# Kernel optimization log

Hardware: AMD Instinct MI355X
Metric: run time of the kernel (lower is better)

Reference implementation:

```python
import jax, jax.numpy as jnp
import numpy as np
from jax import lax

EPS = 1e-5
B = 512

def _conv(x, w, pad):
    # x: [B,Cin,H,W], w: [Cout,Cin,kh,kw]
    return lax.conv_general_dilated(x, w, (1, 1), [(pad, pad), (pad, pad)],
                                    dimension_numbers=('NCHW', 'OIHW', 'NCHW'))

def _bn2d(x, g, b, m, v):
    s = g * lax.rsqrt(v + EPS)
    return x * s[None, :, None, None] + (b - m * s)[None, :, None, None]

def _bn1d(x, g, b, m, v):
    s = g * lax.rsqrt(v + EPS)
    return x * s + (b - m * s)

def _pool2(x):
    return lax.reduce_window(x, -jnp.inf, lax.max, (1, 1, 2, 2), (1, 1, 2, 2), 'VALID')

def setup_inputs() -> dict:
    key = jax.random.key(0)
    ks = iter(jax.random.split(key, 64))
    rn = lambda shape, s=1.0: jax.random.normal(next(ks), shape, dtype=jnp.float32) * s
    un = lambda shape: jax.random.uniform(next(ks), shape, dtype=jnp.float32, minval=0.5, maxval=1.5)
    def bn_params(c):
        return (jnp.ones((c,), jnp.float32), jnp.zeros((c,), jnp.float32), rn((c,), 0.1), un((c,)))
    inp = {"x": rn((B, 3, 64, 64))}
    inp["w1"] = rn((32, 3, 5, 5), 0.1)
    inp["bn1_g"], inp["bn1_b"], inp["bn1_m"], inp["bn1_v"] = bn_params(32)
    inp["w2"] = rn((64, 32, 3, 3), 0.06)
    inp["bn2_g"], inp["bn2_b"], inp["bn2_m"], inp["bn2_v"] = bn_params(64)
    inp["w3"] = rn((128, 64, 3, 3), 0.04)
    inp["bn3_g"], inp["bn3_b"], inp["bn3_m"], inp["bn3_v"] = bn_params(128)
    inp["fc_w"] = rn((256, 8192), 0.01)
    inp["fc_b"] = jnp.zeros((256,), jnp.float32)
    inp["bnf_g"], inp["bnf_b"], inp["bnf_m"], inp["bnf_v"] = bn_params(256)
    inp["c_w1"] = rn((64, 256), 0.06)
    inp["c_b1"] = jnp.zeros((64,), jnp.float32)
    inp["bnc_g"], inp["bnc_b"], inp["bnc_m"], inp["bnc_v"] = bn_params(64)
    inp["c_w2"] = rn((1, 64), 0.1)
    inp["c_b2"] = jnp.zeros((1,), jnp.float32)
    inp["m_w1"] = rn((64, 256), 0.06)
    inp["m_b1"] = jnp.zeros((64,), jnp.float32)
    inp["bnm_g"], inp["bnm_b"], inp["bnm_m"], inp["bnm_v"] = bn_params(64)
    inp["m_w2"] = rn((1, 64), 0.1)
    inp["m_b2"] = jnp.zeros((1,), jnp.float32)
    return inp

def reference(x, w1, bn1_g, bn1_b, bn1_m, bn1_v,
              w2, bn2_g, bn2_b, bn2_m, bn2_v,
              w3, bn3_g, bn3_b, bn3_m, bn3_v,
              fc_w, fc_b, bnf_g, bnf_b, bnf_m, bnf_v,
              c_w1, c_b1, bnc_g, bnc_b, bnc_m, bnc_v, c_w2, c_b2,
              m_w1, m_b1, bnm_g, bnm_b, bnm_m, bnm_v, m_w2, m_b2):
    # Block 1: conv5x5(3->32) + BN + ReLU + maxpool2 -> [B,32,32,32]
    h = _pool2(jax.nn.relu(_bn2d(_conv(x, w1, 2), bn1_g, bn1_b, bn1_m, bn1_v)))
    # Block 2: conv3x3(32->64) + BN + ReLU + maxpool2 -> [B,64,16,16]
    h = _pool2(jax.nn.relu(_bn2d(_conv(h, w2, 1), bn2_g, bn2_b, bn2_m, bn2_v)))
    # Block 3: conv3x3(64->128) + BN + ReLU + maxpool2 + ToDense -> [B,128,8,8]
    h = _pool2(jax.nn.relu(_bn2d(_conv(h, w3, 1), bn3_g, bn3_b, bn3_m, bn3_v)))
    f = h.reshape(h.shape[0], -1)  # [B, 8192]
    s = jax.nn.relu(_bn1d(f @ fc_w.T + fc_b, bnf_g, bnf_b, bnf_m, bnf_v))  # [B,256]
    c = jax.nn.relu(_bn1d(s @ c_w1.T + c_b1, bnc_g, bnc_b, bnc_m, bnc_v)) @ c_w2.T + c_b2
    mo = jax.nn.relu(_bn1d(s @ m_w1.T + m_b1, bnm_g, bnm_b, bnm_m, bnm_v)) @ m_w2.T + m_b2
    return (c, mo)  # ([B,1], [B,1])
```

## Files before the change

kernel.cpp:

```cpp
#include <hip/hip_runtime.h>
#include <hip/hip_bf16.h>

#define EPS 1e-5f

typedef __attribute__((ext_vector_type(8))) short bf16x8;
typedef __attribute__((ext_vector_type(4))) float f32x4;

__device__ __forceinline__ ushort f2b(float f) {
    return __builtin_bit_cast(ushort, __float2bfloat16(f));
}
__device__ __forceinline__ bf16x8 ld_frag(const char* p) {
    return __builtin_bit_cast(bf16x8, *reinterpret_cast<const uint4*>(p));
}

__global__ __launch_bounds__(256) void k_prep_all(
    const float* __restrict__ w1, const float* __restrict__ w2,
    const float* __restrict__ w3, const float* __restrict__ fcw,
    const float* __restrict__ x,
    ushort* __restrict__ w1p, ushort* __restrict__ w2p, ushort* __restrict__ w3p,
    ushort* __restrict__ fcwp, ushort* __restrict__ x4p,
    ushort* __restrict__ h1p, ushort* __restrict__ h2p)
{
    __shared__ ushort l[128 * 66];
    const int bid = blockIdx.x, t = threadIdx.x;
    if (bid < 128) {
        const int total = 5120 + 18432 + 73728;
        for (int i = bid * 256 + t; i < total; i += 128 * 256) {
            if (i < 5120) {
                const int ky = i >> 10, co = (i >> 5) & 31, k = i & 31;
                const int kx = k >> 2, ci = k & 3;
                float v = 0.f;
                if (kx < 5 && ci < 3) v = w1[((co * 3 + ci) * 5 + ky) * 5 + kx];
                w1p[i] = f2b(v);
            } else if (i < 5120 + 18432) {
                const int j = i - 5120;
                const int tap = j >> 11, co = (j >> 5) & 63, ci = j & 31;
                w2p[j] = f2b(w2[(co * 32 + ci) * 9 + tap]);
            } else {
                const int j = i - (5120 + 18432);
                const int tap = j >> 13, co = (j >> 6) & 127, ci = j & 63;
                w3p[j] = f2b(w3[(co * 64 + ci) * 9 + tap]);
            }
        }
    } else if (bid < 384) {
        const int j = bid - 128;
        const float* src = fcw + (size_t)j * 8192;
        #pragma unroll
        for (int i = 0; i < 32; ++i) {
            const int idx = i * 256 + t;
            const int c = idx >> 6, p = idx & 63;
            l[c * 66 + p] = f2b(src[idx]);
        }
        __syncthreads();
        ushort* dst = fcwp + (size_t)j * 8192;
        #pragma unroll
        for (int i = 0; i < 32; ++i) {
            const int idx = i * 256 + t;
            const int c = idx & 127, p = idx >> 7;
            dst[idx] = l[c * 66 + p];
        }
    } else if (bid < 4480) {
        for (int p = (bid - 384) * 256 + t; p < 2506752; p += 4096 * 256) {
            const int n = p / 4896;
            const int rem = p - n * 4896;
            const int row = rem / 72, col = rem - row * 72;
            const int gr = row - 2, gc = col - 2;
            ushort4 pk; pk.x = 0; pk.y = 0; pk.z = 0; pk.w = 0;
            if ((unsigned)gr < 64u && (unsigned)gc < 64u) {
                const size_t base = ((size_t)n * 3 << 12) + (gr << 6) + gc;
                pk.x = f2b(x[base]); pk.y = f2b(x[base + 4096]); pk.z = f2b(x[base + 8192]);
            }
            *reinterpret_cast<ushort4*>(&x4p[(size_t)p * 4]) = pk;
        }
    } else if (bid < 4736) {
        const uint4 z = {0, 0, 0, 0};
        for (int i = (bid - 4480) * 256 + t; i < 270336; i += 256 * 256) {
            const int img = i / 528;
            const int rem = i - img * 528;
            const int px = rem >> 2, gg = rem & 3;
            int row, col;
            if (px < 34)      { row = 0;  col = px; }
            else if (px < 68) { row = 33; col = px - 34; }
            else { const int q = px - 68; row = 1 + (q >> 1); col = (q & 1) ? 33 : 0; }
            *reinterpret_cast<uint4*>(&h1p[(((size_t)img * 34 + row) * 34 + col) * 32 + gg * 8]) = z;
        }
    } else if (bid < 4992) {
        const uint4 z = {0, 0, 0, 0};
        for (int i = (bid - 4736) * 256 + t; i < 278528; i += 256 * 256) {
            const int img = i / 544;
            const int rem = i - img * 544;
            const int px = rem >> 3, gg = rem & 7;
            int row, col;
            if (px < 18)      { row = 0;  col = px; }
            else if (px < 36) { row = 17; col = px - 18; }
            else { const int q = px - 36; row = 1 + (q >> 1); col = (q & 1) ? 17 : 0; }
            *reinterpret_cast<uint4*>(&h2p[(((size_t)img * 18 + row) * 18 + col) * 64 + gg * 8]) = z;
        }
    }
}

__global__ __launch_bounds__(256) void k_conv1(
    const ushort* __restrict__ x4p, const ushort* __restrict__ w1p,
    const float* __restrict__ bg, const float* __restrict__ bb,
    const float* __restrict__ bm, const float* __restrict__ bv,
    ushort* __restrict__ h1p)
{
    __shared__ __align__(16) ushort xs[12 * 72 * 4];
    __shared__ __align__(16) ushort ws[5 * 32 * 32];
    const int bid = blockIdx.x;
    const int n = bid >> 3, q = bid & 7;
    const int t = threadIdx.x;
    const int wave = t >> 6, lane = t & 63;
    const int g = lane >> 4, l15 = lane & 15;

    {
        const ushort* src = x4p + ((size_t)(n * 68 + 8 * q) * 72) * 4;
        for (int i = t; i < 432; i += 256)
            *reinterpret_cast<uint4*>(&xs[i * 8]) = *reinterpret_cast<const uint4*>(src + i * 8);
    }
    for (int i = t; i < 640; i += 256) {
        const int gg = i & 3, r = i >> 2;
        const int co = r & 31;
        const uint4 v = *reinterpret_cast<const uint4*>(&w1p[r * 32 + gg * 8]);
        *reinterpret_cast<uint4*>((char*)ws + r * 64 + ((gg ^ ((co >> 1) & 3)) << 4)) = v;
    }
    __syncthreads();

    f32x4 acc[8][2];
    #pragma unroll
    for (int i = 0; i < 8; ++i) { acc[i][0] = (f32x4){0,0,0,0}; acc[i][1] = (f32x4){0,0,0,0}; }

    const char* xsb = (const char*)xs;
    const char* wsb = (const char*)ws;
    #pragma unroll
    for (int ky = 0; ky < 5; ++ky) {
        bf16x8 a[8], b[2];
        #pragma unroll
        for (int mt = 0; mt < 8; ++mt) {
            const int crl = 2 * wave + (mt >> 2);
            const int ccl = (mt & 3) * 16 + l15;
            const int off = ((crl + ky) * 72 + ccl) * 8 + g * 16;
            const uint2 lo = *reinterpret_cast<const uint2*>(xsb + off);
            const uint2 hi = *reinterpret_cast<const uint2*>(xsb + off + 8);
            uint4 all; all.x = lo.x; all.y = lo.y; all.z = hi.x; all.w = hi.y;
            a[mt] = __builtin_bit_cast(bf16x8, all);
        }
        #pragma unroll
        for (int nt = 0; nt < 2; ++nt) {
            const int co = nt * 16 + l15;
            b[nt] = ld_frag(wsb + (ky * 32 + co) * 64 + ((g ^ ((co >> 1) & 3)) << 4));
        }
        #pragma unroll
        for (int mt = 0; mt < 8; ++mt)
            #pragma unroll
            for (int nt = 0; nt < 2; ++nt)
                acc[mt][nt] = __builtin_amdgcn_mfma_f32_16x16x32_bf16(a[mt], b[nt], acc[mt][nt], 0, 0, 0);
    }

    const int prow = q * 4 + wave;
    #pragma unroll
    for (int nt = 0; nt < 2; ++nt) {
        const int co = nt * 16 + l15;
        const float s = bg[co] * rsqrtf(bv[co] + EPS);
        const float bsv = bb[co] - bm[co] * s;
        #pragma unroll
        for (int mt = 0; mt < 4; ++mt) {
            #pragma unroll
            for (int j = 0; j < 2; ++j) {
                const float v0 = fmaxf(fmaf(acc[mt][nt][2 * j],     s, bsv), 0.f);
                const float v1 = fmaxf(fmaf(acc[mt][nt][2 * j + 1], s, bsv), 0.f);
                const float v2 = fmaxf(fmaf(acc[mt + 4][nt][2 * j],     s, bsv), 0.f);
                const float v3 = fmaxf(fmaf(acc[mt + 4][nt][2 * j + 1], s, bsv), 0.f);
                const int ppc = mt * 8 + g * 2 + j;
                h1p[(((size_t)n * 34 + prow + 1) * 34 + ppc + 1) * 32 + co] =
                    f2b(fmaxf(fmaxf(v0, v1), fmaxf(v2, v3)));
            }
        }
    }
}

__global__ __launch_bounds__(256, 2) void k_conv2(
    const ushort* __restrict__ h1p, const ushort* __restrict__ w2p,
    const float* __restrict__ bg, const float* __restrict__ bb,
    const float* __restrict__ bm, const float* __restrict__ bv,
    ushort* __restrict__ h2p)
{
    __shared__ __align__(16) ushort xs[10 * 34 * 32];
    __shared__ __align__(16) ushort ws[9 * 64 * 32];
    const int bid = blockIdx.x;
    const int ngrp = bid >> 2, q = bid & 3;
    const int t = threadIdx.x;
    const int wave = t >> 6, lane = t & 63;
    const int g = lane >> 4, l15 = lane & 15;
    const char* xsb = (const char*)xs;
    const char* wsb = (const char*)ws;

    for (int i = t; i < 2304; i += 256) {
        const int gg = i & 3, r = i >> 2;
        const int co = r & 63;
        const uint4 v = *reinterpret_cast<const uint4*>(&w2p[r * 32 + gg * 8]);
        *reinterpret_cast<uint4*>((char*)ws + r * 64 + ((gg ^ ((co >> 1) & 3)) << 4)) = v;
    }

    for (int img = 0; img < 4; ++img) {
        const int n = ngrp * 4 + img;
        if (img) __syncthreads();
        {
            const ushort* src = h1p + ((size_t)(n * 34 + 8 * q) * 34) * 32;
            for (int i = t; i < 1360; i += 256) {
                const int gg = i & 3, pix = i >> 2;
                const uint4 v = *reinterpret_cast<const uint4*>(src + i * 8);
                *reinterpret_cast<uint4*>((char*)xs + pix * 64 + ((gg ^ ((pix >> 1) & 3)) << 4)) = v;
            }
        }
        __syncthreads();

        f32x4 acc[4][4];
        #pragma unroll
        for (int i = 0; i < 4; ++i)
            #pragma unroll
            for (int j = 0; j < 4; ++j) acc[i][j] = (f32x4){0,0,0,0};

        #pragma unroll
        for (int tap = 0; tap < 9; ++tap) {
            const int ky = tap / 3, kx = tap - 3 * ky;
            bf16x8 a[4], b[4];
            #pragma unroll
            for (int mt = 0; mt < 4; ++mt) {
                const int crl = 2 * wave + (mt >> 1);
                const int ccl = (mt & 1) * 16 + l15;
                const int pix = (crl + ky) * 34 + ccl + kx;
                a[mt] = ld_frag(xsb + pix * 64 + ((g ^ ((pix >> 1) & 3)) << 4));
            }
            #pragma unroll
            for (int nt = 0; nt < 4; ++nt) {
                const int co = nt * 16 + l15;
                b[nt] = ld_frag(wsb + (tap * 64 + co) * 64 + ((g ^ ((co >> 1) & 3)) << 4));
            }
            #pragma unroll
            for (int mt = 0; mt < 4; ++mt)
                #pragma unroll
                for (int nt = 0; nt < 4; ++nt)
                    acc[mt][nt] = __builtin_amdgcn_mfma_f32_16x16x32_bf16(a[mt], b[nt], acc[mt][nt], 0, 0, 0);
        }

        const int prow = q * 4 + wave;
        #pragma unroll
        for (int nt = 0; nt < 4; ++nt) {
            const int co = nt * 16 + l15;
            const float s = bg[co] * rsqrtf(bv[co] + EPS);
            const float bsv = bb[co] - bm[co] * s;
            #pragma unroll
            for (int mtl = 0; mtl < 2; ++mtl) {
                #pragma unroll
                for (int j = 0; j < 2; ++j) {
                    const float v0 = fmaxf(fmaf(acc[mtl][nt][2 * j],     s, bsv), 0.f);
                    const float v1 = fmaxf(fmaf(acc[mtl][nt][2 * j + 1], s, bsv), 0.f);
                    const float v2 = fmaxf(fmaf(acc[mtl + 2][nt][2 * j],     s, bsv), 0.f);
                    const float v3 = fmaxf(fmaf(acc[mtl + 2][nt][2 * j + 1], s, bsv), 0.f);
                    const int ppc = mtl * 8 + g * 2 + j;
                    h2p[(((size_t)n * 18 + prow + 1) * 18 + ppc + 1) * 64 + co] =
                        f2b(fmaxf(fmaxf(v0, v1), fmaxf(v2, v3)));
                }
            }
        }
    }
}

__global__ __launch_bounds__(256, 2) void k_conv3(
    const ushort* __restrict__ h2p, const ushort* __restrict__ w3p,
    const float* __restrict__ bg, const float* __restrict__ bb,
    const float* __restrict__ bm, const float* __restrict__ bv,
    ushort* __restrict__ h3)
{
    __shared__ __align__(16) ushort xs[2 * 324 * 32];
    __shared__ __align__(16) ushort ws[9 * 64 * 32];
    const int bid = blockIdx.x;
    const int ngrp = bid >> 1, ch = bid & 1;
    const int t = threadIdx.x;
    const int wave = t >> 6, lane = t & 63;
    const int wl = wave & 1, imgw = wave >> 1;
    const int n = ngrp * 2 + imgw;
    const int g = lane >> 4, l15 = lane & 15;
    const char* xsb = (const char*)xs;
    const char* wsb = (const char*)ws;

    f32x4 acc[8][4];
    #pragma unroll
    for (int i = 0; i < 8; ++i)
        #pragma unroll
        for (int j = 0; j < 4; ++j) acc[i][j] = (f32x4){0,0,0,0};

    for (int gci = 0; gci < 2; ++gci) {
        if (gci) __syncthreads();
        for (int i = t; i < 2592; i += 256) {
            const int img2 = i / 1296;
            const int rem = i - img2 * 1296;
            const int pix = rem >> 2, gg = rem & 3;
            const int nsrc = ngrp * 2 + img2;
            const uint4 v = *reinterpret_cast<const uint4*>(
                &h2p[((size_t)nsrc * 324 + pix) * 64 + gci * 32 + gg * 8]);
            *reinterpret_cast<uint4*>((char*)xs + img2 * 20736 + pix * 64 +
                                      ((gg ^ ((pix >> 1) & 3)) << 4)) = v;
        }
        for (int i = t; i < 2304; i += 256) {
            const int gg = i & 3, r = i >> 2;
            const int tap = r >> 6, co = r & 63;
            const uint4 v = *reinterpret_cast<const uint4*>(
                &w3p[((size_t)(tap * 128 + ch * 64 + co) << 6) + gci * 32 + gg * 8]);
            *reinterpret_cast<uint4*>((char*)ws + r * 64 + ((gg ^ ((co >> 1) & 3)) << 4)) = v;
        }
        __syncthreads();
        #pragma unroll
        for (int tap = 0; tap < 9; ++tap) {
            const int ky = tap / 3, kx = tap - 3 * ky;
            bf16x8 a[8], b[4];
            #pragma unroll
            for (int mt = 0; mt < 8; ++mt) {
                const int pr = 8 * wl + mt;
                const int pix = (pr + ky) * 18 + l15 + kx;
                a[mt] = ld_frag(xsb + imgw * 20736 + pix * 64 + ((g ^ ((pix >> 1) & 3)) << 4));
            }
            #pragma unroll
            for (int nt = 0; nt < 4; ++nt) {
                const int co = nt * 16 + l15;
                b[nt] = ld_frag(wsb + (tap * 64 + co) * 64 + ((g ^ ((co >> 1) & 3)) << 4));
            }
            #pragma unroll
            for (int mt = 0; mt < 8; ++mt)
                #pragma unroll
                for (int nt = 0; nt < 4; ++nt)
                    acc[mt][nt] = __builtin_amdgcn_mfma_f32_16x16x32_bf16(a[mt], b[nt], acc[mt][nt], 0, 0, 0);
        }
    }

    #pragma unroll
    for (int nt = 0; nt < 4; ++nt) {
        const int co = ch * 64 + nt * 16 + l15;
        const float s = bg[co] * rsqrtf(bv[co] + EPS);
        const float bsv = bb[co] - bm[co] * s;
        #pragma unroll
        for (int k = 0; k < 4; ++k) {
            #pragma unroll
            for (int j = 0; j < 2; ++j) {
                const float v0 = fmaxf(fmaf(acc[2 * k][nt][2 * j],     s, bsv), 0.f);
                const float v1 = fmaxf(fmaf(acc[2 * k][nt][2 * j + 1], s, bsv), 0.f);
                const float v2 = fmaxf(fmaf(acc[2 * k + 1][nt][2 * j],     s, bsv), 0.f);
                const float v3 = fmaxf(fmaf(acc[2 * k + 1][nt][2 * j + 1], s, bsv), 0.f);
                const int ppr = 4 * wl + k;
                const int pcol = g * 2 + j;
                h3[(((size_t)n * 8 + ppr) * 8 + pcol) * 128 + co] =
                    f2b(fmaxf(fmaxf(v0, v1), fmaxf(v2, v3)));
            }
        }
    }
}

__global__ __launch_bounds__(256) void k_fc(
    const ushort* __restrict__ A, const ushort* __restrict__ Bw, float* __restrict__ C)
{
    __shared__ __align__(16) ushort As[64 * 32];
    __shared__ __align__(16) ushort Bs[64 * 32];
    const int bm = blockIdx.x, bn = blockIdx.y, kz = blockIdx.z;
    const int t = threadIdx.x;
    const int wave = t >> 6, lane = t & 63;
    const int g = lane >> 4, l15 = lane & 15;

    f32x4 acc[4];
    #pragma unroll
    for (int i = 0; i < 4; ++i) acc[i] = (f32x4){0,0,0,0};

    const char* asb = (const char*)As;
    const char* bsb = (const char*)Bs;
    for (int kk = 0; kk < 16; ++kk) {
        const int k0 = kz * 512 + kk * 32;
        if (kk) __syncthreads();
        {
            const int gg = t & 3, row = t >> 2;
            const uint4 va = *reinterpret_cast<const uint4*>(
                &A[(size_t)(bm * 64 + row) * 8192 + k0 + gg * 8]);
            *reinterpret_cast<uint4*>((char*)As + row * 64 + ((gg ^ ((row >> 1) & 3)) << 4)) = va;
            const uint4 vb = *reinterpret_cast<const uint4*>(
                &Bw[(size_t)(bn * 64 + row) * 8192 + k0 + gg * 8]);
            *reinterpret_cast<uint4*>((char*)Bs + row * 64 + ((gg ^ ((row >> 1) & 3)) << 4)) = vb;
        }
        __syncthreads();
        bf16x8 a[4], b;
        #pragma unroll
        for (int mt = 0; mt < 4; ++mt) {
            const int r = mt * 16 + l15;
            a[mt] = ld_frag(asb + r * 64 + ((g ^ ((r >> 1) & 3)) << 4));
        }
        {
            const int r = wave * 16 + l15;
            b = ld_frag(bsb + r * 64 + ((g ^ ((r >> 1) & 3)) << 4));
        }
        #pragma unroll
        for (int mt = 0; mt < 4; ++mt)
            acc[mt] = __builtin_amdgcn_mfma_f32_16x16x32_bf16(a[mt], b, acc[mt], 0, 0, 0);
    }

    float* Cp = C + (size_t)kz * 512 * 256;
    const int col = bn * 64 + wave * 16 + l15;
    #pragma unroll
    for (int mt = 0; mt < 4; ++mt) {
        #pragma unroll
        for (int r = 0; r < 4; ++r) {
            const int row = bm * 64 + mt * 16 + g * 4 + r;
            Cp[(size_t)row * 256 + col] = acc[mt][r];
        }
    }
}

__global__ __launch_bounds__(128) void k_heads(
    const float* __restrict__ sraw, const float* __restrict__ fcb,
    const float* __restrict__ fg, const float* __restrict__ fb,
    const float* __restrict__ fm, const float* __restrict__ fv,
    const float* __restrict__ cw1, const float* __restrict__ cb1,
    const float* __restrict__ cg, const float* __restrict__ cbb,
    const float* __restrict__ cm, const float* __restrict__ cv,
    const float* __restrict__ cw2, const float* __restrict__ cb2,
    const float* __restrict__ mw1, const float* __restrict__ mb1,
    const float* __restrict__ mg, const float* __restrict__ mbb,
    const float* __restrict__ mm, const float* __restrict__ mv,
    const float* __restrict__ mw2, const float* __restrict__ mb2,
    float* __restrict__ outp)
{
    __shared__ float sv[256];
    const int b = blockIdx.x, t = threadIdx.x;
    for (int k = t; k < 256; k += 128) {
        float val = fcb[k];
        #pragma unroll
        for (int z = 0; z < 16; ++z) val += sraw[(size_t)z * 131072 + b * 256 + k];
        const float s = fg[k] * rsqrtf(fv[k] + EPS);
        sv[k] = fmaxf(fmaf(val, s, fb[k] - fm[k] * s), 0.f);
    }
    __syncthreads();
    const int j = t & 63;
    const bool isM = (t >= 64);
    const float* w1  = isM ? mw1 : cw1;
    const float* b1  = isM ? mb1 : cb1;
    const float* g1  = isM ? mg  : cg;
    const float* bb1 = isM ? mbb : cbb;
    const float* m1  = isM ? mm  : cm;
    const float* v1  = isM ? mv  : cv;
    const float* w2  = isM ? mw2 : cw2;
    const float* b2  = isM ? mb2 : cb2;
    float d = 0.f;
    const float* wr = w1 + j * 256;
    #pragma unroll 8
    for (int k = 0; k < 256; ++k) d = fmaf(sv[k], wr[k], d);
    d += b1[j];
    const float s1 = g1[j] * rsqrtf(v1[j] + EPS);
    d = fmaxf(fmaf(d, s1, bb1[j] - m1[j] * s1), 0.f);
    float prod = d * w2[j];
    #pragma unroll
    for (int off = 32; off > 0; off >>= 1) prod += __shfl_down(prod, off);
    if (j == 0) outp[(isM ? 512 : 0) + b] = prod + b2[0];
}

extern "C" void kernel_launch(void* const* d_in, const int* in_sizes, int n_in,
                              void* d_out, int out_size, void* d_ws, size_t ws_size,
                              hipStream_t stream)
{
    const float* x    = (const float*)d_in[0];
    const float* w1   = (const float*)d_in[1];
    const float* bn1g = (const float*)d_in[2];
    const float* bn1b = (const float*)d_in[3];
    const float* bn1m = (const float*)d_in[4];
    const float* bn1v = (const float*)d_in[5];
    const float* w2   = (const float*)d_in[6];
    const float* bn2g = (const float*)d_in[7];
    const float* bn2b = (const float*)d_in[8];
    const float* bn2m = (const float*)d_in[9];
    const float* bn2v = (const float*)d_in[10];
    const float* w3   = (const float*)d_in[11];
    const float* bn3g = (const float*)d_in[12];
    const float* bn3b = (const float*)d_in[13];
    const float* bn3m = (const float*)d_in[14];
    const float* bn3v = (const float*)d_in[15];
    const float* fcw  = (const float*)d_in[16];
    const float* fcb  = (const float*)d_in[17];
    const float* bnfg = (const float*)d_in[18];
    const float* bnfb = (const float*)d_in[19];
    const float* bnfm = (const float*)d_in[20];
    const float* bnfv = (const float*)d_in[21];
    const float* cw1  = (const float*)d_in[22];
    const float* cb1  = (const float*)d_in[23];
    const float* bncg = (const float*)d_in[24];
    const float* bncb = (const float*)d_in[25];
    const float* bncm = (const float*)d_in[26];
    const float* bncv = (const float*)d_in[27];
    const float* cw2  = (const float*)d_in[28];
    const float* cb2  = (const float*)d_in[29];
    const float* mw1  = (const float*)d_in[30];
    const float* mb1  = (const float*)d_in[31];
    const float* bnmg = (const float*)d_in[32];
    const float* bnmb = (const float*)d_in[33];
    const float* bnmm = (const float*)d_in[34];
    const float* bnmv = (const float*)d_in[35];
    const float* mw2  = (const float*)d_in[36];
    const float* mb2  = (const float*)d_in[37];

    char* W = (char*)d_ws;
    ushort* x4p  = (ushort*)(W);
    ushort* h1p  = (ushort*)(W + 20054016);
    ushort* h2p  = (ushort*)(W + 57933824);
    ushort* h3   = (ushort*)(W + 79167488);
    ushort* w1p  = (ushort*)(W + 87556096);
    ushort* w2p  = (ushort*)(W + 87566336);
    ushort* w3p  = (ushort*)(W + 87603200);
    ushort* fcwp = (ushort*)(W + 87750656);
    float*  sr   = (float*) (W + 91944960);
    float* outp = (float*)d_out;

    k_prep_all<<<4992, 256, 0, stream>>>(w1, w2, w3, fcw, x,
                                         w1p, w2p, w3p, fcwp, x4p, h1p, h2p);
    k_conv1<<<512 * 8, 256, 0, stream>>>(x4p, w1p, bn1g, bn1b, bn1m, bn1v, h1p);
    k_conv2<<<128 * 4, 256, 0, stream>>>(h1p, w2p, bn2g, bn2b, bn2m, bn2v, h2p);
    k_conv3<<<256 * 2, 256, 0, stream>>>(h2p, w3p, bn3g, bn3b, bn3m, bn3v, h3);
    k_fc<<<dim3(8, 4, 16), 256, 0, stream>>>(h3, fcwp, sr);
    k_heads<<<512, 128, 0, stream>>>(sr, fcb, bnfg, bnfb, bnfm, bnfv,
                                     cw1, cb1, bncg, bncb, bncm, bncv, cw2, cb2,
                                     mw1, mb1, bnmg, bnmb, bnmm, bnmv, mw2, mb2, outp);
}
```

Before: 261.2 us.

## Drop LDS staging in conv kernels and load MFMA fragments from global

The three convolution kernels no longer stage input tiles and weights in shared memory. Each wave now loads its MFMA A and B fragments straight from global memory and relies on L1/L2 caching for reuse. conv2 and conv3 are restructured to handle one image per block, launching 4x and 2x more blocks, and launch bounds are raised to allow more resident blocks. This removes the LDS copy and barrier overhead in exchange for redundant global/cache traffic and possibly uncoalesced fragment loads.

```diff
diff --git a/kernel.cpp b/kernel.cpp
--- a/kernel.cpp
+++ b/kernel.cpp
@@ -9,7 +9,7 @@
 __device__ __forceinline__ ushort f2b(float f) {
     return __builtin_bit_cast(ushort, __float2bfloat16(f));
 }
-__device__ __forceinline__ bf16x8 ld_frag(const char* p) {
+__device__ __forceinline__ bf16x8 ld_frag(const void* p) {
     return __builtin_bit_cast(bf16x8, *reinterpret_cast<const uint4*>(p));
 }
 
@@ -99,56 +99,35 @@
     }
 }
 
-__global__ __launch_bounds__(256) void k_conv1(
+__global__ __launch_bounds__(256, 3) void k_conv1(
     const ushort* __restrict__ x4p, const ushort* __restrict__ w1p,
     const float* __restrict__ bg, const float* __restrict__ bb,
     const float* __restrict__ bm, const float* __restrict__ bv,
     ushort* __restrict__ h1p)
 {
-    __shared__ __align__(16) ushort xs[12 * 72 * 4];
-    __shared__ __align__(16) ushort ws[5 * 32 * 32];
     const int bid = blockIdx.x;
     const int n = bid >> 3, q = bid & 7;
     const int t = threadIdx.x;
     const int wave = t >> 6, lane = t & 63;
     const int g = lane >> 4, l15 = lane & 15;
 
-    {
-        const ushort* src = x4p + ((size_t)(n * 68 + 8 * q) * 72) * 4;
-        for (int i = t; i < 432; i += 256)
-            *reinterpret_cast<uint4*>(&xs[i * 8]) = *reinterpret_cast<const uint4*>(src + i * 8);
-    }
-    for (int i = t; i < 640; i += 256) {
-        const int gg = i & 3, r = i >> 2;
-        const int co = r & 31;
-        const uint4 v = *reinterpret_cast<const uint4*>(&w1p[r * 32 + gg * 8]);
-        *reinterpret_cast<uint4*>((char*)ws + r * 64 + ((gg ^ ((co >> 1) & 3)) << 4)) = v;
-    }
-    __syncthreads();
-
     f32x4 acc[8][2];
     #pragma unroll
     for (int i = 0; i < 8; ++i) { acc[i][0] = (f32x4){0,0,0,0}; acc[i][1] = (f32x4){0,0,0,0}; }
 
-    const char* xsb = (const char*)xs;
-    const char* wsb = (const char*)ws;
     #pragma unroll
     for (int ky = 0; ky < 5; ++ky) {
         bf16x8 a[8], b[2];
         #pragma unroll
         for (int mt = 0; mt < 8; ++mt) {
-            const int crl = 2 * wave + (mt >> 2);
-            const int ccl = (mt & 3) * 16 + l15;
-            const int off = ((crl + ky) * 72 + ccl) * 8 + g * 16;
-            const uint2 lo = *reinterpret_cast<const uint2*>(xsb + off);
-            const uint2 hi = *reinterpret_cast<const uint2*>(xsb + off + 8);
-            uint4 all; all.x = lo.x; all.y = lo.y; all.z = hi.x; all.w = hi.y;
-            a[mt] = __builtin_bit_cast(bf16x8, all);
+            const int cr = 8 * q + 2 * wave + (mt >> 2) + ky;
+            const int px = (mt & 3) * 16 + l15 + 2 * g;
+            a[mt] = ld_frag(&x4p[(((size_t)n * 68 + cr) * 72 + px) * 4]);
         }
         #pragma unroll
         for (int nt = 0; nt < 2; ++nt) {
             const int co = nt * 16 + l15;
-            b[nt] = ld_frag(wsb + (ky * 32 + co) * 64 + ((g ^ ((co >> 1) & 3)) << 4));
+            b[nt] = ld_frag(&w1p[(ky * 32 + co) * 32 + g * 8]);
         }
         #pragma unroll
         for (int mt = 0; mt < 8; ++mt)
@@ -179,63 +158,102 @@
     }
 }
 
-__global__ __launch_bounds__(256, 2) void k_conv2(
+__global__ __launch_bounds__(256, 4) void k_conv2(
     const ushort* __restrict__ h1p, const ushort* __restrict__ w2p,
     const float* __restrict__ bg, const float* __restrict__ bb,
     const float* __restrict__ bm, const float* __restrict__ bv,
     ushort* __restrict__ h2p)
 {
-    __shared__ __align__(16) ushort xs[10 * 34 * 32];
-    __shared__ __align__(16) ushort ws[9 * 64 * 32];
     const int bid = blockIdx.x;
-    const int ngrp = bid >> 2, q = bid & 3;
+    const int n = bid >> 2, q = bid & 3;
     const int t = threadIdx.x;
     const int wave = t >> 6, lane = t & 63;
     const int g = lane >> 4, l15 = lane & 15;
-    const char* xsb = (const char*)xs;
-    const char* wsb = (const char*)ws;
-
-    for (int i = t; i < 2304; i += 256) {
-        const int gg = i & 3, r = i >> 2;
-        const int co = r & 63;
-        const uint4 v = *reinterpret_cast<const uint4*>(&w2p[r * 32 + gg * 8]);
-        *reinterpret_cast<uint4*>((char*)ws + r * 64 + ((gg ^ ((co >> 1) & 3)) << 4)) = v;
-    }
-
-    for (int img = 0; img < 4; ++img) {
-        const int n = ngrp * 4 + img;
-        if (img) __syncthreads();
-        {
-            const ushort* src = h1p + ((size_t)(n * 34 + 8 * q) * 34) * 32;
-            for (int i = t; i < 1360; i += 256) {
-                const int gg = i & 3, pix = i >> 2;
-                const uint4 v = *reinterpret_cast<const uint4*>(src + i * 8);
-                *reinterpret_cast<uint4*>((char*)xs + pix * 64 + ((gg ^ ((pix >> 1) & 3)) << 4)) = v;
-            }
-        }
-        __syncthreads();
-
-        f32x4 acc[4][4];
-        #pragma unroll
-        for (int i = 0; i < 4; ++i)
-            #pragma unroll
-            for (int j = 0; j < 4; ++j) acc[i][j] = (f32x4){0,0,0,0};
-
+
+    f32x4 acc[4][4];
+    #pragma unroll
+    for (int i = 0; i < 4; ++i)
+        #pragma unroll
+        for (int j = 0; j < 4; ++j) acc[i][j] = (f32x4){0,0,0,0};
+
+    #pragma unroll
+    for (int tap = 0; tap < 9; ++tap) {
+        const int ky = tap / 3, kx = tap - 3 * ky;
+        bf16x8 a[4], b[4];
+        #pragma unroll
+        for (int mt = 0; mt < 4; ++mt) {
+            const int row = 8 * q + 2 * wave + (mt >> 1) + ky;
+            const int col = (mt & 1) * 16 + l15 + kx;
+            a[mt] = ld_frag(&h1p[(((size_t)n * 34 + row) * 34 + col) * 32 + g * 8]);
+        }
+        #pragma unroll
+        for (int nt = 0; nt < 4; ++nt) {
+            const int co = nt * 16 + l15;
+            b[nt] = ld_frag(&w2p[(tap * 64 + co) * 32 + g * 8]);
+        }
+        #pragma unroll
+        for (int mt = 0; mt < 4; ++mt)
+            #pragma unroll
+            for (int nt = 0; nt < 4; ++nt)
+                acc[mt][nt] = __builtin_amdgcn_mfma_f32_16x16x32_bf16(a[mt], b[nt], acc[mt][nt], 0, 0, 0);
+    }
+
+    const int prow = q * 4 + wave;
+    #pragma unroll
+    for (int nt = 0; nt < 4; ++nt) {
+        const int co = nt * 16 + l15;
+        const float s = bg[co] * rsqrtf(bv[co] + EPS);
+        const float bsv = bb[co] - bm[co] * s;
+        #pragma unroll
+        for (int mtl = 0; mtl < 2; ++mtl) {
+            #pragma unroll
+            for (int j = 0; j < 2; ++j) {
+                const float v0 = fmaxf(fmaf(acc[mtl][nt][2 * j],     s, bsv), 0.f);
+                const float v1 = fmaxf(fmaf(acc[mtl][nt][2 * j + 1], s, bsv), 0.f);
+                const float v2 = fmaxf(fmaf(acc[mtl + 2][nt][2 * j],     s, bsv), 0.f);
+                const float v3 = fmaxf(fmaf(acc[mtl + 2][nt][2 * j + 1], s, bsv), 0.f);
+                const int ppc = mtl * 8 + g * 2 + j;
+                h2p[(((size_t)n * 18 + prow + 1) * 18 + ppc + 1) * 64 + co] =
+                    f2b(fmaxf(fmaxf(v0, v1), fmaxf(v2, v3)));
+            }
+        }
+    }
+}
+
+__global__ __launch_bounds__(256, 4) void k_conv3(
+    const ushort* __restrict__ h2p, const ushort* __restrict__ w3p,
+    const float* __restrict__ bg, const float* __restrict__ bb,
+    const float* __restrict__ bm, const float* __restrict__ bv,
+    ushort* __restrict__ h3)
+{
+    const int bid = blockIdx.x;
+    const int n = bid >> 1, ch = bid & 1;
+    const int t = threadIdx.x;
+    const int wave = t >> 6, lane = t & 63;
+    const int g = lane >> 4, l15 = lane & 15;
+
+    f32x4 acc[4][4];
+    #pragma unroll
+    for (int i = 0; i < 4; ++i)
+        #pragma unroll
+        for (int j = 0; j < 4; ++j) acc[i][j] = (f32x4){0,0,0,0};
+
+    #pragma unroll
+    for (int gci = 0; gci < 2; ++gci) {
         #pragma unroll
         for (int tap = 0; tap < 9; ++tap) {
             const int ky = tap / 3, kx = tap - 3 * ky;
             bf16x8 a[4], b[4];
             #pragma unroll
             for (int mt = 0; mt < 4; ++mt) {
-                const int crl = 2 * wave + (mt >> 1);
-                const int ccl = (mt & 1) * 16 + l15;
-                const int pix = (crl + ky) * 34 + ccl + kx;
-                a[mt] = ld_frag(xsb + pix * 64 + ((g ^ ((pix >> 1) & 3)) << 4));
+                const int row = 4 * wave + mt + ky;
+                const int col = l15 + kx;
+                a[mt] = ld_frag(&h2p[(((size_t)n * 18 + row) * 18 + col) * 64 + gci * 32 + g * 8]);
             }
             #pragma unroll
             for (int nt = 0; nt < 4; ++nt) {
-                const int co = nt * 16 + l15;
-                b[nt] = ld_frag(wsb + (tap * 64 + co) * 64 + ((g ^ ((co >> 1) & 3)) << 4));
+                const int co = ch * 64 + nt * 16 + l15;
+                b[nt] = ld_frag(&w3p[((size_t)(tap * 128 + co)) * 64 + gci * 32 + g * 8]);
             }
             #pragma unroll
             for (int mt = 0; mt < 4; ++mt)
@@ -243,95 +261,6 @@
                 for (int nt = 0; nt < 4; ++nt)
                     acc[mt][nt] = __builtin_amdgcn_mfma_f32_16x16x32_bf16(a[mt], b[nt], acc[mt][nt], 0, 0, 0);
         }
-
-        const int prow = q * 4 + wave;
-        #pragma unroll
-        for (int nt = 0; nt < 4; ++nt) {
-            const int co = nt * 16 + l15;
-            const float s = bg[co] * rsqrtf(bv[co] + EPS);
-            const float bsv = bb[co] - bm[co] * s;
-            #pragma unroll
-            for (int mtl = 0; mtl < 2; ++mtl) {
-                #pragma unroll
-                for (int j = 0; j < 2; ++j) {
-                    const float v0 = fmaxf(fmaf(acc[mtl][nt][2 * j],     s, bsv), 0.f);
-                    const float v1 = fmaxf(fmaf(acc[mtl][nt][2 * j + 1], s, bsv), 0.f);
-                    const float v2 = fmaxf(fmaf(acc[mtl + 2][nt][2 * j],     s, bsv), 0.f);
-                    const float v3 = fmaxf(fmaf(acc[mtl + 2][nt][2 * j + 1], s, bsv), 0.f);
-                    const int ppc = mtl * 8 + g * 2 + j;
-                    h2p[(((size_t)n * 18 + prow + 1) * 18 + ppc + 1) * 64 + co] =
-                        f2b(fmaxf(fmaxf(v0, v1), fmaxf(v2, v3)));
-                }
-            }
-        }
-    }
-}
-
-__global__ __launch_bounds__(256, 2) void k_conv3(
-    const ushort* __restrict__ h2p, const ushort* __restrict__ w3p,
-    const float* __restrict__ bg, const float* __restrict__ bb,
-    const float* __restrict__ bm, const float* __restrict__ bv,
-    ushort* __restrict__ h3)
-{
-    __shared__ __align__(16) ushort xs[2 * 324 * 32];
-    __shared__ __align__(16) ushort ws[9 * 64 * 32];
-    const int bid = blockIdx.x;
-    const int ngrp = bid >> 1, ch = bid & 1;
-    const int t = threadIdx.x;
-    const int wave = t >> 6, lane = t & 63;
-    const int wl = wave & 1, imgw = wave >> 1;
-    const int n = ngrp * 2 + imgw;
-    const int g = lane >> 4, l15 = lane & 15;
-    const char* xsb = (const char*)xs;
-    const char* wsb = (const char*)ws;
-
-    f32x4 acc[8][4];
-    #pragma unroll
-    for (int i = 0; i < 8; ++i)
-        #pragma unroll
-        for (int j = 0; j < 4; ++j) acc[i][j] = (f32x4){0,0,0,0};
-
-    for (int gci = 0; gci < 2; ++gci) {
-        if (gci) __syncthreads();
-        for (int i = t; i < 2592; i += 256) {
-            const int img2 = i / 1296;
-            const int rem = i - img2 * 1296;
-            const int pix = rem >> 2, gg = rem & 3;
-            const int nsrc = ngrp * 2 + img2;
-            const uint4 v = *reinterpret_cast<const uint4*>(
-                &h2p[((size_t)nsrc * 324 + pix) * 64 + gci * 32 + gg * 8]);
-            *reinterpret_cast<uint4*>((char*)xs + img2 * 20736 + pix * 64 +
-                                      ((gg ^ ((pix >> 1) & 3)) << 4)) = v;
-        }
-        for (int i = t; i < 2304; i += 256) {
-            const int gg = i & 3, r = i >> 2;
-            const int tap = r >> 6, co = r & 63;
-            const uint4 v = *reinterpret_cast<const uint4*>(
-                &w3p[((size_t)(tap * 128 + ch * 64 + co) << 6) + gci * 32 + gg * 8]);
-            *reinterpret_cast<uint4*>((char*)ws + r * 64 + ((gg ^ ((co >> 1) & 3)) << 4)) = v;
-        }
-        __syncthreads();
-        #pragma unroll
-        for (int tap = 0; tap < 9; ++tap) {
-            const int ky = tap / 3, kx = tap - 3 * ky;
-            bf16x8 a[8], b[4];
-            #pragma unroll
-            for (int mt = 0; mt < 8; ++mt) {
-                const int pr = 8 * wl + mt;
-                const int pix = (pr + ky) * 18 + l15 + kx;
-                a[mt] = ld_frag(xsb + imgw * 20736 + pix * 64 + ((g ^ ((pix >> 1) & 3)) << 4));
-            }
-            #pragma unroll
-            for (int nt = 0; nt < 4; ++nt) {
-                const int co = nt * 16 + l15;
-                b[nt] = ld_frag(wsb + (tap * 64 + co) * 64 + ((g ^ ((co >> 1) & 3)) << 4));
-            }
-            #pragma unroll
-            for (int mt = 0; mt < 8; ++mt)
-                #pragma unroll
-                for (int nt = 0; nt < 4; ++nt)
-                    acc[mt][nt] = __builtin_amdgcn_mfma_f32_16x16x32_bf16(a[mt], b[nt], acc[mt][nt], 0, 0, 0);
-        }
     }
 
     #pragma unroll
@@ -340,14 +269,14 @@
         const float s = bg[co] * rsqrtf(bv[co] + EPS);
         const float bsv = bb[co] - bm[co] * s;
         #pragma unroll
-        for (int k = 0; k < 4; ++k) {
+        for (int k = 0; k < 2; ++k) {
             #pragma unroll
             for (int j = 0; j < 2; ++j) {
                 const float v0 = fmaxf(fmaf(acc[2 * k][nt][2 * j],     s, bsv), 0.f);
                 const float v1 = fmaxf(fmaf(acc[2 * k][nt][2 * j + 1], s, bsv), 0.f);
                 const float v2 = fmaxf(fmaf(acc[2 * k + 1][nt][2 * j],     s, bsv), 0.f);
                 const float v3 = fmaxf(fmaf(acc[2 * k + 1][nt][2 * j + 1], s, bsv), 0.f);
-                const int ppr = 4 * wl + k;
+                const int ppr = 2 * wave + k;
                 const int pcol = g * 2 + j;
                 h3[(((size_t)n * 8 + ppr) * 8 + pcol) * 128 + co] =
                     f2b(fmaxf(fmaxf(v0, v1), fmaxf(v2, v3)));
@@ -517,8 +446,8 @@
     k_prep_all<<<4992, 256, 0, stream>>>(w1, w2, w3, fcw, x,
                                          w1p, w2p, w3p, fcwp, x4p, h1p, h2p);
     k_conv1<<<512 * 8, 256, 0, stream>>>(x4p, w1p, bn1g, bn1b, bn1m, bn1v, h1p);
-    k_conv2<<<128 * 4, 256, 0, stream>>>(h1p, w2p, bn2g, bn2b, bn2m, bn2v, h2p);
-    k_conv3<<<256 * 2, 256, 0, stream>>>(h2p, w3p, bn3g, bn3b, bn3m, bn3v, h3);
+    k_conv2<<<512 * 4, 256, 0, stream>>>(h1p, w2p, bn2g, bn2b, bn2m, bn2v, h2p);
+    k_conv3<<<512 * 2, 256, 0, stream>>>(h2p, w3p, bn3g, bn3b, bn3m, bn3v, h3);
     k_fc<<<dim3(8, 4, 16), 256, 0, stream>>>(h3, fcwp, sr);
     k_heads<<<512, 128, 0, stream>>>(sr, fcb, bnfg, bnfb, bnfm, bnfv,
                                      cw1, cb1, bncg, bncb, bncm, bncv, cw2, cb2,
```

Measured after the change: 337.9 us. +29.4%, slower.

## Split conv2 and conv3 work to one image per block for more parallelism

Applied to the files above, without the earlier changes.

conv2 now processes a single image per block instead of looping over four, and conv3 handles one image per block instead of two, with its accumulator tile halved. Grid sizes grow accordingly (2048 and 1024 blocks) and the min-blocks launch bound is dropped. The intent is to fill more CUs and lower per-thread register pressure on the wide GPU. The cost is reloading the shared-memory weight tiles per block, which means more global weight traffic and more setup overhead per image.

```diff
diff --git a/kernel.cpp b/kernel.cpp
--- a/kernel.cpp
+++ b/kernel.cpp
@@ -9,7 +9,7 @@
 __device__ __forceinline__ ushort f2b(float f) {
     return __builtin_bit_cast(ushort, __float2bfloat16(f));
 }
-__device__ __forceinline__ bf16x8 ld_frag(const char* p) {
+__device__ __forceinline__ bf16x8 ld_frag(const void* p) {
     return __builtin_bit_cast(bf16x8, *reinterpret_cast<const uint4*>(p));
 }
 
@@ -179,7 +179,7 @@
     }
 }
 
-__global__ __launch_bounds__(256, 2) void k_conv2(
+__global__ __launch_bounds__(256) void k_conv2(
     const ushort* __restrict__ h1p, const ushort* __restrict__ w2p,
     const float* __restrict__ bg, const float* __restrict__ bb,
     const float* __restrict__ bm, const float* __restrict__ bv,
@@ -188,7 +188,7 @@
     __shared__ __align__(16) ushort xs[10 * 34 * 32];
     __shared__ __align__(16) ushort ws[9 * 64 * 32];
     const int bid = blockIdx.x;
-    const int ngrp = bid >> 2, q = bid & 3;
+    const int n = bid >> 2, q = bid & 3;
     const int t = threadIdx.x;
     const int wave = t >> 6, lane = t & 63;
     const int g = lane >> 4, l15 = lane & 15;
@@ -201,107 +201,96 @@
         const uint4 v = *reinterpret_cast<const uint4*>(&w2p[r * 32 + gg * 8]);
         *reinterpret_cast<uint4*>((char*)ws + r * 64 + ((gg ^ ((co >> 1) & 3)) << 4)) = v;
     }
-
-    for (int img = 0; img < 4; ++img) {
-        const int n = ngrp * 4 + img;
-        if (img) __syncthreads();
-        {
-            const ushort* src = h1p + ((size_t)(n * 34 + 8 * q) * 34) * 32;
-            for (int i = t; i < 1360; i += 256) {
-                const int gg = i & 3, pix = i >> 2;
-                const uint4 v = *reinterpret_cast<const uint4*>(src + i * 8);
-                *reinterpret_cast<uint4*>((char*)xs + pix * 64 + ((gg ^ ((pix >> 1) & 3)) << 4)) = v;
-            }
-        }
-        __syncthreads();
-
-        f32x4 acc[4][4];
-        #pragma unroll
-        for (int i = 0; i < 4; ++i)
-            #pragma unroll
-            for (int j = 0; j < 4; ++j) acc[i][j] = (f32x4){0,0,0,0};
-
-        #pragma unroll
-        for (int tap = 0; tap < 9; ++tap) {
-            const int ky = tap / 3, kx = tap - 3 * ky;
-            bf16x8 a[4], b[4];
-            #pragma unroll
-            for (int mt = 0; mt < 4; ++mt) {
-                const int crl = 2 * wave + (mt >> 1);
-                const int ccl = (mt & 1) * 16 + l15;
-                const int pix = (crl + ky) * 34 + ccl + kx;
-                a[mt] = ld_frag(xsb + pix * 64 + ((g ^ ((pix >> 1) & 3)) << 4));
-            }
-            #pragma unroll
-            for (int nt = 0; nt < 4; ++nt) {
-                const int co = nt * 16 + l15;
-                b[nt] = ld_frag(wsb + (tap * 64 + co) * 64 + ((g ^ ((co >> 1) & 3)) << 4));
-            }
-            #pragma unroll
-            for (int mt = 0; mt < 4; ++mt)
-                #pragma unroll
-                for (int nt = 0; nt < 4; ++nt)
-                    acc[mt][nt] = __builtin_amdgcn_mfma_f32_16x16x32_bf16(a[mt], b[nt], acc[mt][nt], 0, 0, 0);
-        }
-
-        const int prow = q * 4 + wave;
+    {
+        const ushort* src = h1p + ((size_t)(n * 34 + 8 * q) * 34) * 32;
+        for (int i = t; i < 1360; i += 256) {
+            const int gg = i & 3, pix = i >> 2;
+            const uint4 v = *reinterpret_cast<const uint4*>(src + i * 8);
+            *reinterpret_cast<uint4*>((char*)xs + pix * 64 + ((gg ^ ((pix >> 1) & 3)) << 4)) = v;
+        }
+    }
+    __syncthreads();
+
+    f32x4 acc[4][4];
+    #pragma unroll
+    for (int i = 0; i < 4; ++i)
+        #pragma unroll
+        for (int j = 0; j < 4; ++j) acc[i][j] = (f32x4){0,0,0,0};
+
+    #pragma unroll
+    for (int tap = 0; tap < 9; ++tap) {
+        const int ky = tap / 3, kx = tap - 3 * ky;
+        bf16x8 a[4], b[4];
+        #pragma unroll
+        for (int mt = 0; mt < 4; ++mt) {
+            const int crl = 2 * wave + (mt >> 1);
+            const int ccl = (mt & 1) * 16 + l15;
+            const int pix = (crl + ky) * 34 + ccl + kx;
+            a[mt] = ld_frag(xsb + pix * 64 + ((g ^ ((pix >> 1) & 3)) << 4));
+        }
         #pragma unroll
         for (int nt = 0; nt < 4; ++nt) {
             const int co = nt * 16 + l15;
-            const float s = bg[co] * rsqrtf(bv[co] + EPS);
-            const float bsv = bb[co] - bm[co] * s;
-            #pragma unroll
-            for (int mtl = 0; mtl < 2; ++mtl) {
-                #pragma unroll
-                for (int j = 0; j < 2; ++j) {
-                    const float v0 = fmaxf(fmaf(acc[mtl][nt][2 * j],     s, bsv), 0.f);
-                    const float v1 = fmaxf(fmaf(acc[mtl][nt][2 * j + 1], s, bsv), 0.f);
-                    const float v2 = fmaxf(fmaf(acc[mtl + 2][nt][2 * j],     s, bsv), 0.f);
-                    const float v3 = fmaxf(fmaf(acc[mtl + 2][nt][2 * j + 1], s, bsv), 0.f);
-                    const int ppc = mtl * 8 + g * 2 + j;
-                    h2p[(((size_t)n * 18 + prow + 1) * 18 + ppc + 1) * 64 + co] =
-                        f2b(fmaxf(fmaxf(v0, v1), fmaxf(v2, v3)));
-                }
-            }
-        }
-    }
-}
-
-__global__ __launch_bounds__(256, 2) void k_conv3(
+            b[nt] = ld_frag(wsb + (tap * 64 + co) * 64 + ((g ^ ((co >> 1) & 3)) << 4));
+        }
+        #pragma unroll
+        for (int mt = 0; mt < 4; ++mt)
+            #pragma unroll
+            for (int nt = 0; nt < 4; ++nt)
+                acc[mt][nt] = __builtin_amdgcn_mfma_f32_16x16x32_bf16(a[mt], b[nt], acc[mt][nt], 0, 0, 0);
+    }
+
+    const int prow = q * 4 + wave;
+    #pragma unroll
+    for (int nt = 0; nt < 4; ++nt) {
+        const int co = nt * 16 + l15;
+        const float s = bg[co] * rsqrtf(bv[co] + EPS);
+        const float bsv = bb[co] - bm[co] * s;
+        #pragma unroll
+        for (int mtl = 0; mtl < 2; ++mtl) {
+            #pragma unroll
+            for (int j = 0; j < 2; ++j) {
+                const float v0 = fmaxf(fmaf(acc[mtl][nt][2 * j],     s, bsv), 0.f);
+                const float v1 = fmaxf(fmaf(acc[mtl][nt][2 * j + 1], s, bsv), 0.f);
+                const float v2 = fmaxf(fmaf(acc[mtl + 2][nt][2 * j],     s, bsv), 0.f);
+                const float v3 = fmaxf(fmaf(acc[mtl + 2][nt][2 * j + 1], s, bsv), 0.f);
+                const int ppc = mtl * 8 + g * 2 + j;
+                h2p[(((size_t)n * 18 + prow + 1) * 18 + ppc + 1) * 64 + co] =
+                    f2b(fmaxf(fmaxf(v0, v1), fmaxf(v2, v3)));
+            }
+        }
+    }
+}
+
+__global__ __launch_bounds__(256) void k_conv3(
     const ushort* __restrict__ h2p, const ushort* __restrict__ w3p,
     const float* __restrict__ bg, const float* __restrict__ bb,
     const float* __restrict__ bm, const float* __restrict__ bv,
     ushort* __restrict__ h3)
 {
-    __shared__ __align__(16) ushort xs[2 * 324 * 32];
+    __shared__ __align__(16) ushort xs[324 * 32];
     __shared__ __align__(16) ushort ws[9 * 64 * 32];
     const int bid = blockIdx.x;
-    const int ngrp = bid >> 1, ch = bid & 1;
+    const int n = bid >> 1, ch = bid & 1;
     const int t = threadIdx.x;
     const int wave = t >> 6, lane = t & 63;
-    const int wl = wave & 1, imgw = wave >> 1;
-    const int n = ngrp * 2 + imgw;
     const int g = lane >> 4, l15 = lane & 15;
     const char* xsb = (const char*)xs;
     const char* wsb = (const char*)ws;
 
-    f32x4 acc[8][4];
-    #pragma unroll
-    for (int i = 0; i < 8; ++i)
+    f32x4 acc[4][4];
+    #pragma unroll
+    for (int i = 0; i < 4; ++i)
         #pragma unroll
         for (int j = 0; j < 4; ++j) acc[i][j] = (f32x4){0,0,0,0};
 
     for (int gci = 0; gci < 2; ++gci) {
         if (gci) __syncthreads();
-        for (int i = t; i < 2592; i += 256) {
-            const int img2 = i / 1296;
-            const int rem = i - img2 * 1296;
-            const int pix = rem >> 2, gg = rem & 3;
-            const int nsrc = ngrp * 2 + img2;
+        for (int i = t; i < 1296; i += 256) {
+            const int gg = i & 3, pix = i >> 2;
             const uint4 v = *reinterpret_cast<const uint4*>(
-                &h2p[((size_t)nsrc * 324 + pix) * 64 + gci * 32 + gg * 8]);
-            *reinterpret_cast<uint4*>((char*)xs + img2 * 20736 + pix * 64 +
-                                      ((gg ^ ((pix >> 1) & 3)) << 4)) = v;
+                &h2p[((size_t)n * 324 + pix) * 64 + gci * 32 + gg * 8]);
+            *reinterpret_cast<uint4*>((char*)xs + pix * 64 + ((gg ^ ((pix >> 1) & 3)) << 4)) = v;
         }
         for (int i = t; i < 2304; i += 256) {
             const int gg = i & 3, r = i >> 2;
@@ -314,12 +303,12 @@
         #pragma unroll
         for (int tap = 0; tap < 9; ++tap) {
             const int ky = tap / 3, kx = tap - 3 * ky;
-            bf16x8 a[8], b[4];
-            #pragma unroll
-            for (int mt = 0; mt < 8; ++mt) {
-                const int pr = 8 * wl + mt;
+            bf16x8 a[4], b[4];
+            #pragma unroll
+            for (int mt = 0; mt < 4; ++mt) {
+                const int pr = 4 * wave + mt;
                 const int pix = (pr + ky) * 18 + l15 + kx;
-                a[mt] = ld_frag(xsb + imgw * 20736 + pix * 64 + ((g ^ ((pix >> 1) & 3)) << 4));
+                a[mt] = ld_frag(xsb + pix * 64 + ((g ^ ((pix >> 1) & 3)) << 4));
             }
             #pragma unroll
             for (int nt = 0; nt < 4; ++nt) {
@@ -327,7 +316,7 @@
                 b[nt] = ld_frag(wsb + (tap * 64 + co) * 64 + ((g ^ ((co >> 1) & 3)) << 4));
             }
             #pragma unroll
-            for (int mt = 0; mt < 8; ++mt)
+            for (int mt = 0; mt < 4; ++mt)
                 #pragma unroll
                 for (int nt = 0; nt < 4; ++nt)
                     acc[mt][nt] = __builtin_amdgcn_mfma_f32_16x16x32_bf16(a[mt], b[nt], acc[mt][nt], 0, 0, 0);
@@ -340,14 +329,15 @@
         const float s = bg[co] * rsqrtf(bv[co] + EPS);
         const float bsv = bb[co] - bm[co] * s;
         #pragma unroll
-        for (int k = 0; k < 4; ++k) {
+        for (int mtl = 0; mtl < 2; ++mtl) {
             #pragma unroll
             for (int j = 0; j < 2; ++j) {
-                const float v0 = fmaxf(fmaf(acc[2 * k][nt][2 * j],     s, bsv), 0.f);
-                const float v1 = fmaxf(fmaf(acc[2 * k][nt][2 * j + 1], s, bsv), 0.f);
-                const float v2 = fmaxf(fmaf(acc[2 * k + 1][nt][2 * j],     s, bsv), 0.f);
-                const float v3 = fmaxf(fmaf(acc[2 * k + 1][nt][2 * j + 1], s, bsv), 0.f);
-                const int ppr = 4 * wl + k;
+                const int mt = mtl * 2;
+                const float v0 = fmaxf(fmaf(acc[mt][nt][2 * j],     s, bsv), 0.f);
+                const float v1 = fmaxf(fmaf(acc[mt][nt][2 * j + 1], s, bsv), 0.f);
+                const float v2 = fmaxf(fmaf(acc[mt + 1][nt][2 * j],     s, bsv), 0.f);
+                const float v3 = fmaxf(fmaf(acc[mt + 1][nt][2 * j + 1], s, bsv), 0.f);
+                const int ppr = 2 * wave + mtl;
                 const int pcol = g * 2 + j;
                 h3[(((size_t)n * 8 + ppr) * 8 + pcol) * 128 + co] =
                     f2b(fmaxf(fmaxf(v0, v1), fmaxf(v2, v3)));
@@ -517,8 +507,8 @@
     k_prep_all<<<4992, 256, 0, stream>>>(w1, w2, w3, fcw, x,
                                          w1p, w2p, w3p, fcwp, x4p, h1p, h2p);
     k_conv1<<<512 * 8, 256, 0, stream>>>(x4p, w1p, bn1g, bn1b, bn1m, bn1v, h1p);
-    k_conv2<<<128 * 4, 256, 0, stream>>>(h1p, w2p, bn2g, bn2b, bn2m, bn2v, h2p);
-    k_conv3<<<256 * 2, 256, 0, stream>>>(h2p, w3p, bn3g, bn3b, bn3m, bn3v, h3);
+    k_conv2<<<512 * 4, 256, 0, stream>>>(h1p, w2p, bn2g, bn2b, bn2m, bn2v, h2p);
+    k_conv3<<<512 * 2, 256, 0, stream>>>(h2p, w3p, bn3g, bn3b, bn3m, bn3v, h3);
     k_fc<<<dim3(8, 4, 16), 256, 0, stream>>>(h3, fcwp, sr);
     k_heads<<<512, 128, 0, stream>>>(sr, fcb, bnfg, bnfb, bnfm, bnfv,
                                      cw1, cb1, bncg, bncb, bncm, bncv, cw2, cb2,
```

New measurement: 250.0 us. 1.04x faster.
